# Kernel tuning notes

Measured on AMD Instinct MI355X. Metric: run time of the kernel, lower is better.

The kernel has to match this reference:

```python
import jax, jax.numpy as jnp
import numpy as np

HIDDEN = 1024
FEAT = 2048
BOTTLENECK = 512
B, T = 64, 512


def setup_inputs() -> dict:
    key = jax.random.key(0)
    k1, k2, k3, k4, k5 = jax.random.split(key, 5)
    hidden = jax.random.normal(k1, (B, HIDDEN), dtype=jnp.float32)
    feats = jax.random.normal(k2, (B, T, FEAT), dtype=jnp.float32)
    # nn.Linear weights stored as [out, in]; apply as x @ W.T
    W = jax.random.normal(k3, (BOTTLENECK, HIDDEN), dtype=jnp.float32) * (1.0 / np.sqrt(HIDDEN))
    U = jax.random.normal(k4, (BOTTLENECK, FEAT), dtype=jnp.float32) * (1.0 / np.sqrt(FEAT))
    b = jnp.ones((BOTTLENECK,), dtype=jnp.float32)
    w = jax.random.normal(k5, (1, BOTTLENECK), dtype=jnp.float32) * (1.0 / np.sqrt(BOTTLENECK))
    return {"hidden": hidden, "feats": feats, "W": W, "U": U, "b": b, "w": w}


def reference(hidden, feats, W, U, b, w):
    Wh = hidden @ W.T                      # [B, K]
    Uv = jnp.einsum('btf,kf->btk', feats, U)  # [B, T, K]
    e = jnp.tanh(Wh[:, None, :] + Uv + b)  # [B, T, K]
    energies = jnp.einsum('btk,ok->bto', e, w)  # [B, T, 1]
    weights = jax.nn.softmax(energies, axis=1)  # softmax over time
    attn_feats = jnp.sum(feats * weights, axis=1)  # [B, F]
    return attn_feats, weights
```

## Files before the change

kernel.cpp:

```cpp
#include <hip/hip_runtime.h>
#include <math.h>

#define BATCH 64
#define TDIM 512
#define FEAT 2048
#define HID 1024
#define KDIM 512
#define MROWS (BATCH * TDIM)
#define TCH 16
#define TCLEN (TDIM / TCH)

#define NSTEP (FEAT / 64)
#define TSLOT 2048
#define ASLOTS (128 * 32 * TSLOT)
#define BSLOTS (2 * 32 * TSLOT)

typedef __attribute__((ext_vector_type(8))) short short8;
typedef __attribute__((ext_vector_type(4))) float floatx4;

#define GLL16(g, l)                                                     \
    __builtin_amdgcn_global_load_lds(                                   \
        (const __attribute__((address_space(1))) void*)(g),             \
        (__attribute__((address_space(3))) void*)(l), 16, 0, 0)

#define VMWAIT(N) asm volatile("s_waitcnt vmcnt(" #N ")" ::: "memory")
#define SCHEDB    __builtin_amdgcn_sched_barrier(0)
#define SBAR      __builtin_amdgcn_s_barrier()

__device__ __forceinline__ unsigned short f2bf(float x) {
    unsigned int u = __float_as_uint(x);
    u += 0x7FFFu + ((u >> 16) & 1u);
    return (unsigned short)(u >> 16);
}

__global__ __launch_bounds__(256) void k0p(const float* __restrict__ feats,
                                           const float* __restrict__ U,
                                           const float* __restrict__ hidden,
                                           const float* __restrict__ W,
                                           const float* __restrict__ bias,
                                           unsigned short* __restrict__ Apk,
                                           unsigned short* __restrict__ Bpk,
                                           float* __restrict__ whb) {
    int bx = blockIdx.x;
    if (bx < 8192) {
        for (size_t gsl = (size_t)bx * 256 + threadIdx.x; gsl < ASLOTS;
             gsl += (size_t)8192 * 256) {
            int strip = (int)(gsl >> 16);
            int rem   = (int)(gsl & 65535);
            int tile  = rem >> 11;
            int s     = rem & 2047;
            int r     = s >> 3;
            int c     = (s & 7) ^ (r & 7);
            const float* src = feats + ((size_t)strip * 256 + r) * FEAT + tile * 64 + c * 8;
            float4 v0 = *(const float4*)src;
            float4 v1 = *(const float4*)(src + 4);
            ushort4 o0, o1;
            o0.x = f2bf(v0.x); o0.y = f2bf(v0.y); o0.z = f2bf(v0.z); o0.w = f2bf(v0.w);
            o1.x = f2bf(v1.x); o1.y = f2bf(v1.y); o1.z = f2bf(v1.z); o1.w = f2bf(v1.w);
            ((ushort4*)Apk)[gsl * 2]     = o0;
            ((ushort4*)Apk)[gsl * 2 + 1] = o1;
        }
    } else if (bx < 8704) {
        size_t gsl = (size_t)(bx - 8192) * 256 + threadIdx.x;
        int cb   = (int)(gsl >> 16);
        int rem  = (int)(gsl & 65535);
        int tile = rem >> 11;
        int s    = rem & 2047;
        int r    = s >> 3;
        int c    = (s & 7) ^ (r & 7);
        const float* src = U + ((size_t)cb * 256 + r) * FEAT + tile * 64 + c * 8;
        float4 v0 = *(const float4*)src;
        float4 v1 = *(const float4*)(src + 4);
        ushort4 o0, o1;
        o0.x = f2bf(v0.x); o0.y = f2bf(v0.y); o0.z = f2bf(v0.z); o0.w = f2bf(v0.w);
        o1.x = f2bf(v1.x); o1.y = f2bf(v1.y); o1.z = f2bf(v1.z); o1.w = f2bf(v1.w);
        ((ushort4*)Bpk)[gsl * 2]     = o0;
        ((ushort4*)Bpk)[gsl * 2 + 1] = o1;
    } else {
        int bid = bx - 8704;
        int b = bid >> 7;
        int k = (bid & 127) * 4 + (threadIdx.x >> 6);
        int lane = threadIdx.x & 63;
        const float* hrow = hidden + (size_t)b * HID;
        const float* wrow = W + (size_t)k * HID;
        float acc = 0.f;
        #pragma unroll 4
        for (int h = lane; h < HID; h += 64) acc += hrow[h] * wrow[h];
        #pragma unroll
        for (int off = 32; off > 0; off >>= 1) acc += __shfl_down(acc, off, 64);
        if (lane == 0) whb[b * KDIM + k] = acc + bias[k];
    }
}

__global__ __launch_bounds__(512, 2) void k2p(const unsigned short* __restrict__ Apk,
                                              const unsigned short* __restrict__ Bpk,
                                              const float* __restrict__ whb,
                                              const float* __restrict__ wvec,
                                              float* __restrict__ partial) {
    __shared__ __align__(16) unsigned short As[2][16384];
    __shared__ __align__(16) unsigned short Bs[2][16384];

    const int tid  = threadIdx.x;
    const int wave = tid >> 6;
    const int lane = tid & 63;
    const int wm = wave >> 2, wn = wave & 3;
    const int col = lane & 15, quad = lane >> 4;
    const int bx = blockIdx.x, by = blockIdx.y;

    const unsigned short* gA = Apk + (size_t)bx * (32 * TSLOT) * 8;
    const unsigned short* gB = Bpk + (size_t)by * (32 * TSLOT) * 8;

    #define STAGE(tt, hh, bb)                                                   \
        do {                                                                    \
            const int sbase_ = ((hh) & 1) * 1024 + wave * 128;                  \
            if ((hh) < 2) {                                                     \
                GLL16(gA + ((size_t)(tt) * TSLOT + sbase_) * 8 + lane * 8,      \
                      &As[bb][sbase_ * 8]);                                     \
                GLL16(gA + ((size_t)(tt) * TSLOT + sbase_ + 64) * 8 + lane * 8, \
                      &As[bb][(sbase_ + 64) * 8]);                              \
            } else {                                                            \
                GLL16(gB + ((size_t)(tt) * TSLOT + sbase_) * 8 + lane * 8,      \
                      &Bs[bb][sbase_ * 8]);                                     \
                GLL16(gB + ((size_t)(tt) * TSLOT + sbase_ + 64) * 8 + lane * 8, \
                      &Bs[bb][(sbase_ + 64) * 8]);                              \
            }                                                                   \
        } while (0)

    floatx4 acc[8][4];
    #pragma unroll
    for (int i = 0; i < 8; ++i)
        #pragma unroll
        for (int j = 0; j < 4; ++j) acc[i][j] = (floatx4){0.f, 0.f, 0.f, 0.f};

    #pragma unroll
    for (int h = 0; h < 4; ++h) STAGE(0, h, 0);

    short8 bf[4][2];
    for (int t = 0; t < NSTEP; ++t) {
        const int cb = t & 1, sb = cb ^ 1;
        #pragma unroll
        for (int p = 0; p < 4; ++p) {
            if (t < NSTEP - 1) STAGE(t + 1, p, sb);
            if (p == 0) {
                if (t < NSTEP - 1) { VMWAIT(2); } else { VMWAIT(0); }
                SCHEDB;
            }
            SBAR; SCHEDB;

            short8 af[2][2];
            #pragma unroll
            for (int i = 0; i < 2; ++i)
                #pragma unroll
                for (int kk = 0; kk < 2; ++kk) {
                    const int row = wm * 128 + (2 * p + i) * 16 + col;
                    af[i][kk] = *(const short8*)
                        &As[cb][(row * 8 + ((kk * 4 + quad) ^ (col & 7))) * 8];
                }
            if (p == 0) {
                #pragma unroll
                for (int j = 0; j < 4; ++j)
                    #pragma unroll
                    for (int kk = 0; kk < 2; ++kk) {
                        const int row = wn * 64 + j * 16 + col;
                        bf[j][kk] = *(const short8*)
                            &Bs[cb][(row * 8 + ((kk * 4 + quad) ^ (col & 7))) * 8];
                    }
            }
            __builtin_amdgcn_s_setprio(1);
            #pragma unroll
            for (int i = 0; i < 2; ++i)
                #pragma unroll
                for (int j = 0; j < 4; ++j)
                    #pragma unroll
                    for (int kk = 0; kk < 2; ++kk)
                        acc[2 * p + i][j] = __builtin_amdgcn_mfma_f32_16x16x32_bf16(
                            af[i][kk], bf[j][kk], acc[2 * p + i][j], 0, 0, 0);
            __builtin_amdgcn_s_setprio(0);
            SCHEDB; SBAR; SCHEDB;
        }
    }
    #undef STAGE

    __syncthreads();

    float (*sums)[256] = (float (*)[256])As;
    const int b = bx >> 1;
    float wk[4], hk[4];
    #pragma unroll
    for (int j = 0; j < 4; ++j) {
        const int k = by * 256 + wn * 64 + j * 16 + col;
        wk[j] = wvec[k];
        hk[j] = whb[b * KDIM + k];
    }
    #pragma unroll
    for (int i = 0; i < 8; ++i) {
        #pragma unroll
        for (int r = 0; r < 4; ++r) {
            float s = 0.f;
            #pragma unroll
            for (int j = 0; j < 4; ++j)
                s += tanhf(acc[i][j][r] + hk[j]) * wk[j];
            #pragma unroll
            for (int off = 8; off > 0; off >>= 1)
                s += __shfl_down(s, off, 16);
            if (col == 0)
                sums[wn][wm * 128 + i * 16 + quad * 4 + r] = s;
        }
    }
    __syncthreads();
    if (tid < 256)
        partial[(size_t)by * MROWS + bx * 256 + tid] =
            sums[0][tid] + sums[1][tid] + sums[2][tid] + sums[3][tid];
}

__global__ __launch_bounds__(512) void k3n(const float* __restrict__ partial,
                                           float* __restrict__ wout) {
    int b = blockIdx.x;
    int t = threadIdx.x;
    int idx = b * TDIM + t;
    float e = partial[idx] + partial[MROWS + idx];

    __shared__ float sm[512];
    sm[t] = e;
    __syncthreads();
    #pragma unroll
    for (int s = 256; s > 0; s >>= 1) {
        if (t < s) sm[t] = fmaxf(sm[t], sm[t + s]);
        __syncthreads();
    }
    float m = sm[0];
    __syncthreads();
    float ex = __expf(e - m);
    sm[t] = ex;
    __syncthreads();
    #pragma unroll
    for (int s = 256; s > 0; s >>= 1) {
        if (t < s) sm[t] += sm[t + s];
        __syncthreads();
    }
    float inv = 1.f / sm[0];
    wout[b * TDIM + t] = ex * inv;
}

__global__ __launch_bounds__(256) void k4p(const unsigned short* __restrict__ Apk,
                                           const float* __restrict__ weights,
                                           float* __restrict__ partial4) {
    int b  = blockIdx.y;
    int t0 = blockIdx.x * TCLEN;
    int tile = threadIdx.x >> 3;
    int ch   = threadIdx.x & 7;
    int f0   = tile * 64 + ch * 8;
    __shared__ float wsm[TCLEN];
    if (threadIdx.x < TCLEN) wsm[threadIdx.x] = weights[b * TDIM + t0 + threadIdx.x];
    __syncthreads();

    float a[8];
    #pragma unroll
    for (int e = 0; e < 8; ++e) a[e] = 0.f;
    #pragma unroll 4
    for (int t = 0; t < TCLEN; ++t) {
        int row = b * TDIM + t0 + t;
        int strip = row >> 8, r = row & 255;
        const short8 v = *(const short8*)(Apk +
            (((size_t)strip * 65536 + (size_t)tile * TSLOT + r * 8 + (ch ^ (r & 7))) * 8));
        float w = wsm[t];
        #pragma unroll
        for (int e = 0; e < 8; ++e)
            a[e] += __uint_as_float(((unsigned int)(unsigned short)v[e]) << 16) * w;
    }
    float* op = partial4 + ((size_t)blockIdx.x * BATCH + b) * FEAT + f0;
    float4 o0 = {a[0], a[1], a[2], a[3]};
    float4 o1 = {a[4], a[5], a[6], a[7]};
    *(float4*)op = o0;
    *(float4*)(op + 4) = o1;
}

__global__ __launch_bounds__(256) void k5_reduce(const float* __restrict__ partial4,
                                                 float* __restrict__ out) {
    int i4 = blockIdx.x * 256 + threadIdx.x;
    float4 s = ((const float4*)partial4)[i4];
    #pragma unroll
    for (int c = 1; c < TCH; ++c) {
        float4 v = ((const float4*)partial4)[(size_t)c * (BATCH * FEAT / 4) + i4];
        s.x += v.x; s.y += v.y; s.z += v.z; s.w += v.w;
    }
    ((float4*)out)[i4] = s;
}

#define BM 128
#define BN 128
#define BF 16
#define LDSPAD 4

__global__ __launch_bounds__(256) void k1_whb(const float* __restrict__ hidden,
                                              const float* __restrict__ W,
                                              const float* __restrict__ bias,
                                              float* __restrict__ whb) {
    int b = blockIdx.y;
    int k = blockIdx.x * 4 + (threadIdx.x >> 6);
    int lane = threadIdx.x & 63;
    const float* hrow = hidden + (size_t)b * HID;
    const float* wrow = W + (size_t)k * HID;
    float acc = 0.f;
    #pragma unroll 4
    for (int h = lane; h < HID; h += 64) acc += hrow[h] * wrow[h];
    #pragma unroll
    for (int off = 32; off > 0; off >>= 1) acc += __shfl_down(acc, off, 64);
    if (lane == 0) whb[b * KDIM + k] = acc + bias[k];
}

__global__ __launch_bounds__(256) void k2_energy(const float* __restrict__ feats,
                                                 const float* __restrict__ U,
                                                 const float* __restrict__ whb,
                                                 const float* __restrict__ wvec,
                                                 float* __restrict__ partial) {
    __shared__ __align__(16) float As[BF][BM + LDSPAD];
    __shared__ __align__(16) float Us[BF][BN + LDSPAD];

    const int row0 = blockIdx.x * BM;
    const int k0   = blockIdx.y * BN;
    const int tid  = threadIdx.x;
    const int tx   = tid & 15;
    const int ty   = tid >> 4;

    float acc[8][8];
    #pragma unroll
    for (int i = 0; i < 8; ++i)
        #pragma unroll
        for (int j = 0; j < 8; ++j) acc[i][j] = 0.f;

    for (int f0 = 0; f0 < FEAT; f0 += BF) {
        #pragma unroll
        for (int l = 0; l < 2; ++l) {
            int li = tid + l * 256;
            int r  = li >> 2;
            int c4 = (li & 3) * 4;
            float4 av = *(const float4*)(feats + (size_t)(row0 + r) * FEAT + f0 + c4);
            float4 uv = *(const float4*)(U     + (size_t)(k0   + r) * FEAT + f0 + c4);
            As[c4 + 0][r] = av.x; As[c4 + 1][r] = av.y;
            As[c4 + 2][r] = av.z; As[c4 + 3][r] = av.w;
            Us[c4 + 0][r] = uv.x; Us[c4 + 1][r] = uv.y;
            Us[c4 + 2][r] = uv.z; Us[c4 + 3][r] = uv.w;
        }
        __syncthreads();
        #pragma unroll
        for (int kf = 0; kf < BF; ++kf) {
            float4 a0 = *(const float4*)&As[kf][ty * 8];
            float4 a1 = *(const float4*)&As[kf][ty * 8 + 4];
            float4 u0 = *(const float4*)&Us[kf][tx * 8];
            float4 u1 = *(const float4*)&Us[kf][tx * 8 + 4];
            float a[8] = {a0.x, a0.y, a0.z, a0.w, a1.x, a1.y, a1.z, a1.w};
            float u[8] = {u0.x, u0.y, u0.z, u0.w, u1.x, u1.y, u1.z, u1.w};
            #pragma unroll
            for (int i = 0; i < 8; ++i)
                #pragma unroll
                for (int j = 0; j < 8; ++j) acc[i][j] += a[i] * u[j];
        }
        __syncthreads();
    }

    const int b = row0 >> 9;
    float psum[8];
    #pragma unroll
    for (int i = 0; i < 8; ++i) {
        float s = 0.f;
        #pragma unroll
        for (int j = 0; j < 8; ++j) {
            int k = k0 + tx * 8 + j;
            s += tanhf(acc[i][j] + whb[b * KDIM + k]) * wvec[k];
        }
        psum[i] = s;
    }
    #pragma unroll
    for (int off = 8; off > 0; off >>= 1)
        #pragma unroll
        for (int i = 0; i < 8; ++i) psum[i] += __shfl_down(psum[i], off, 16);

    if (tx == 0) {
        int c = blockIdx.y;
        #pragma unroll
        for (int i = 0; i < 8; ++i)
            partial[c * MROWS + row0 + ty * 8 + i] = psum[i];
    }
}

__global__ __launch_bounds__(512) void k3_softmax(const float* __restrict__ partial,
                                                  float* __restrict__ wout) {
    int b = blockIdx.x;
    int t = threadIdx.x;
    float e = 0.f;
    #pragma unroll
    for (int c = 0; c < 4; ++c) e += partial[c * MROWS + b * TDIM + t];

    __shared__ float sm[512];
    sm[t] = e;
    __syncthreads();
    #pragma unroll
    for (int s = 256; s > 0; s >>= 1) {
        if (t < s) sm[t] = fmaxf(sm[t], sm[t + s]);
        __syncthreads();
    }
    float m = sm[0];
    __syncthreads();
    float ex = __expf(e - m);
    sm[t] = ex;
    __syncthreads();
    #pragma unroll
    for (int s = 256; s > 0; s >>= 1) {
        if (t < s) sm[t] += sm[t + s];
        __syncthreads();
    }
    float inv = 1.f / sm[0];
    wout[b * TDIM + t] = ex * inv;
}

__global__ __launch_bounds__(256) void k4_direct(const float* __restrict__ feats,
                                                 const float* __restrict__ weights,
                                                 float* __restrict__ out) {
    int b = blockIdx.y;
    int f4 = (blockIdx.x * 256 + threadIdx.x) * 4;
    __shared__ float wsm[TDIM];
    wsm[threadIdx.x]       = weights[b * TDIM + threadIdx.x];
    wsm[threadIdx.x + 256] = weights[b * TDIM + 256 + threadIdx.x];
    __syncthreads();

    const float* fp = feats + (size_t)b * TDIM * FEAT + f4;
    float ax = 0.f, ay = 0.f, az = 0.f, aw = 0.f;
    for (int t = 0; t < TDIM; ++t) {
        float4 v = *(const float4*)(fp + (size_t)t * FEAT);
        float w = wsm[t];
        ax += v.x * w; ay += v.y * w; az += v.z * w; aw += v.w * w;
    }
    float4 o = {ax, ay, az, aw};
    *(float4*)(out + (size_t)b * FEAT + f4) = o;
}

extern "C" void kernel_launch(void* const* d_in, const int* in_sizes, int n_in,
                              void* d_out, int out_size, void* d_ws, size_t ws_size,
                              hipStream_t stream) {
    const float* hidden = (const float*)d_in[0];
    const float* feats  = (const float*)d_in[1];
    const float* W      = (const float*)d_in[2];
    const float* U      = (const float*)d_in[3];
    const float* bias   = (const float*)d_in[4];
    const float* wvec   = (const float*)d_in[5];

    float* out         = (float*)d_out;
    float* attn_out    = out;
    float* weights_out = out + (size_t)BATCH * FEAT;
    float* whb         = weights_out;
    float* partial     = attn_out;

    const size_t aBytes    = (size_t)ASLOTS * 16;
    const size_t bBytes    = (size_t)BSLOTS * 16;
    const size_t poolBytes = (size_t)TCH * BATCH * FEAT * sizeof(float);
    const bool fast = ws_size >= aBytes + bBytes + poolBytes;

    if (fast) {
        unsigned short* Apk = (unsigned short*)d_ws;
        unsigned short* Bpk = (unsigned short*)((char*)d_ws + aBytes);
        float* pool4 = (float*)((char*)d_ws + aBytes + bBytes);
        k0p<<<dim3(16896), 256, 0, stream>>>(feats, U, hidden, W, bias,
                                             Apk, Bpk, whb);
        k2p<<<dim3(128, 2), 512, 0, stream>>>(Apk, Bpk, whb, wvec, partial);
        k3n<<<dim3(BATCH), 512, 0, stream>>>(partial, weights_out);
        k4p<<<dim3(TCH, BATCH), 256, 0, stream>>>(Apk, weights_out, pool4);
        k5_reduce<<<dim3(BATCH * FEAT / 4 / 256), 256, 0, stream>>>(pool4, attn_out);
    } else {
        k1_whb<<<dim3(KDIM / 4, BATCH), 256, 0, stream>>>(hidden, W, bias, whb);
        k2_energy<<<dim3(MROWS / 128, KDIM / 128), 256, 0, stream>>>(
            feats, U, whb, wvec, partial);
        k3_softmax<<<dim3(BATCH), 512, 0, stream>>>(partial, weights_out);
        k4_direct<<<dim3(FEAT / 1024, BATCH), 256, 0, stream>>>(
            feats, weights_out, attn_out);
    }
}
```

Baseline: 532.4 us.

## Shrink energy GEMM tiles to 128x128 and replace partial-sum reduction with atomics

The bf16 packed layout moves from 256-row to 128-row strips, and the energy GEMM goes from a 512-thread 256x256 double-buffered pipelined kernel to a simpler 256-thread 128x128 single-buffered kernel on a 256x4 grid. Energy partials now live in workspace across four K-chunks, and k3n sums all four. The attention-pooling stage drops its separate reduction kernel: k4a atomically adds into the output, which k0p now zeroes. This trades the explicit load/compute overlap and larger reuse for more blocks and one fewer launch, at the cost of exposed load latency, extra B-tile traffic and atomic contention.

```diff
diff --git a/kernel.cpp b/kernel.cpp
--- a/kernel.cpp
+++ b/kernel.cpp
@@ -11,9 +11,9 @@
 #define TCLEN (TDIM / TCH)
 
 #define NSTEP (FEAT / 64)
-#define TSLOT 2048
-#define ASLOTS (128 * 32 * TSLOT)
-#define BSLOTS (2 * 32 * TSLOT)
+#define TSLOT 1024
+#define ASLOTS (256 * 32 * TSLOT)
+#define BSLOTS (4 * 32 * TSLOT)
 
 typedef __attribute__((ext_vector_type(8))) short short8;
 typedef __attribute__((ext_vector_type(4))) float floatx4;
@@ -22,10 +22,6 @@
     __builtin_amdgcn_global_load_lds(                                   \
         (const __attribute__((address_space(1))) void*)(g),             \
         (__attribute__((address_space(3))) void*)(l), 16, 0, 0)
-
-#define VMWAIT(N) asm volatile("s_waitcnt vmcnt(" #N ")" ::: "memory")
-#define SCHEDB    __builtin_amdgcn_sched_barrier(0)
-#define SBAR      __builtin_amdgcn_s_barrier()
 
 __device__ __forceinline__ unsigned short f2bf(float x) {
     unsigned int u = __float_as_uint(x);
@@ -40,18 +36,19 @@
                                            const float* __restrict__ bias,
                                            unsigned short* __restrict__ Apk,
                                            unsigned short* __restrict__ Bpk,
-                                           float* __restrict__ whb) {
+                                           float* __restrict__ whb,
+                                           float* __restrict__ attn_zero) {
     int bx = blockIdx.x;
     if (bx < 8192) {
         for (size_t gsl = (size_t)bx * 256 + threadIdx.x; gsl < ASLOTS;
              gsl += (size_t)8192 * 256) {
-            int strip = (int)(gsl >> 16);
-            int rem   = (int)(gsl & 65535);
-            int tile  = rem >> 11;
-            int s     = rem & 2047;
+            int strip = (int)(gsl >> 15);
+            int rem   = (int)(gsl & 32767);
+            int tile  = rem >> 10;
+            int s     = rem & 1023;
             int r     = s >> 3;
             int c     = (s & 7) ^ (r & 7);
-            const float* src = feats + ((size_t)strip * 256 + r) * FEAT + tile * 64 + c * 8;
+            const float* src = feats + ((size_t)strip * 128 + r) * FEAT + tile * 64 + c * 8;
             float4 v0 = *(const float4*)src;
             float4 v1 = *(const float4*)(src + 4);
             ushort4 o0, o1;
@@ -62,13 +59,13 @@
         }
     } else if (bx < 8704) {
         size_t gsl = (size_t)(bx - 8192) * 256 + threadIdx.x;
-        int cb   = (int)(gsl >> 16);
-        int rem  = (int)(gsl & 65535);
-        int tile = rem >> 11;
-        int s    = rem & 2047;
+        int kb   = (int)(gsl >> 15);
+        int rem  = (int)(gsl & 32767);
+        int tile = rem >> 10;
+        int s    = rem & 1023;
         int r    = s >> 3;
         int c    = (s & 7) ^ (r & 7);
-        const float* src = U + ((size_t)cb * 256 + r) * FEAT + tile * 64 + c * 8;
+        const float* src = U + ((size_t)kb * 128 + r) * FEAT + tile * 64 + c * 8;
         float4 v0 = *(const float4*)src;
         float4 v1 = *(const float4*)(src + 4);
         ushort4 o0, o1;
@@ -76,8 +73,11 @@
         o1.x = f2bf(v1.x); o1.y = f2bf(v1.y); o1.z = f2bf(v1.z); o1.w = f2bf(v1.w);
         ((ushort4*)Bpk)[gsl * 2]     = o0;
         ((ushort4*)Bpk)[gsl * 2 + 1] = o1;
+    } else if (bx < 8832) {
+        int i4 = (bx - 8704) * 256 + threadIdx.x;
+        ((float4*)attn_zero)[i4] = (float4){0.f, 0.f, 0.f, 0.f};
     } else {
-        int bid = bx - 8704;
+        int bid = bx - 8832;
         int b = bid >> 7;
         int k = (bid & 127) * 4 + (threadIdx.x >> 6);
         int lane = threadIdx.x & 63;
@@ -92,108 +92,72 @@
     }
 }
 
-__global__ __launch_bounds__(512, 2) void k2p(const unsigned short* __restrict__ Apk,
-                                              const unsigned short* __restrict__ Bpk,
-                                              const float* __restrict__ whb,
-                                              const float* __restrict__ wvec,
-                                              float* __restrict__ partial) {
-    __shared__ __align__(16) unsigned short As[2][16384];
-    __shared__ __align__(16) unsigned short Bs[2][16384];
+__global__ __launch_bounds__(256) void k2m(const unsigned short* __restrict__ Apk,
+                                           const unsigned short* __restrict__ Bpk,
+                                           const float* __restrict__ whb,
+                                           const float* __restrict__ wvec,
+                                           float* __restrict__ partial) {
+    __shared__ __align__(16) unsigned short As[TSLOT * 8];
+    __shared__ __align__(16) unsigned short Bs[TSLOT * 8];
 
     const int tid  = threadIdx.x;
     const int wave = tid >> 6;
     const int lane = tid & 63;
-    const int wm = wave >> 2, wn = wave & 3;
+    const int wm = wave >> 1, wn = wave & 1;
     const int col = lane & 15, quad = lane >> 4;
-    const int bx = blockIdx.x, by = blockIdx.y;
-
-    const unsigned short* gA = Apk + (size_t)bx * (32 * TSLOT) * 8;
-    const unsigned short* gB = Bpk + (size_t)by * (32 * TSLOT) * 8;
-
-    #define STAGE(tt, hh, bb)                                                   \
-        do {                                                                    \
-            const int sbase_ = ((hh) & 1) * 1024 + wave * 128;                  \
-            if ((hh) < 2) {                                                     \
-                GLL16(gA + ((size_t)(tt) * TSLOT + sbase_) * 8 + lane * 8,      \
-                      &As[bb][sbase_ * 8]);                                     \
-                GLL16(gA + ((size_t)(tt) * TSLOT + sbase_ + 64) * 8 + lane * 8, \
-                      &As[bb][(sbase_ + 64) * 8]);                              \
-            } else {                                                            \
-                GLL16(gB + ((size_t)(tt) * TSLOT + sbase_) * 8 + lane * 8,      \
-                      &Bs[bb][sbase_ * 8]);                                     \
-                GLL16(gB + ((size_t)(tt) * TSLOT + sbase_ + 64) * 8 + lane * 8, \
-                      &Bs[bb][(sbase_ + 64) * 8]);                              \
-            }                                                                   \
-        } while (0)
-
-    floatx4 acc[8][4];
-    #pragma unroll
-    for (int i = 0; i < 8; ++i)
+    const int bx = blockIdx.x;
+    const int kb = blockIdx.y;
+
+    const unsigned short* gA = Apk + ((size_t)bx * (32 * TSLOT) + wave * 256 + lane) * 8;
+    const unsigned short* gB = Bpk + ((size_t)kb * (32 * TSLOT) + wave * 256 + lane) * 8;
+    unsigned short* lA = As + (wave * 256) * 8;
+    unsigned short* lB = Bs + (wave * 256) * 8;
+
+    floatx4 acc[4][4];
+    #pragma unroll
+    for (int i = 0; i < 4; ++i)
         #pragma unroll
         for (int j = 0; j < 4; ++j) acc[i][j] = (floatx4){0.f, 0.f, 0.f, 0.f};
 
-    #pragma unroll
-    for (int h = 0; h < 4; ++h) STAGE(0, h, 0);
-
-    short8 bf[4][2];
     for (int t = 0; t < NSTEP; ++t) {
-        const int cb = t & 1, sb = cb ^ 1;
-        #pragma unroll
-        for (int p = 0; p < 4; ++p) {
-            if (t < NSTEP - 1) STAGE(t + 1, p, sb);
-            if (p == 0) {
-                if (t < NSTEP - 1) { VMWAIT(2); } else { VMWAIT(0); }
-                SCHEDB;
-            }
-            SBAR; SCHEDB;
-
-            short8 af[2][2];
-            #pragma unroll
-            for (int i = 0; i < 2; ++i)
-                #pragma unroll
-                for (int kk = 0; kk < 2; ++kk) {
-                    const int row = wm * 128 + (2 * p + i) * 16 + col;
-                    af[i][kk] = *(const short8*)
-                        &As[cb][(row * 8 + ((kk * 4 + quad) ^ (col & 7))) * 8];
-                }
-            if (p == 0) {
+        #pragma unroll
+        for (int g = 0; g < 4; ++g) {
+            GLL16(gA + (size_t)(t * 1024 + g * 64) * 8, lA + g * 64 * 8);
+            GLL16(gB + (size_t)(t * 1024 + g * 64) * 8, lB + g * 64 * 8);
+        }
+        __syncthreads();
+
+        #pragma unroll
+        for (int kk = 0; kk < 2; ++kk) {
+            const int sw = (kk * 4 + quad) ^ (col & 7);
+            short8 af[4], bf[4];
+            #pragma unroll
+            for (int i = 0; i < 4; ++i)
+                af[i] = *(const short8*)&As[((wm * 64 + i * 16 + col) * 8 + sw) * 8];
+            #pragma unroll
+            for (int j = 0; j < 4; ++j)
+                bf[j] = *(const short8*)&Bs[((wn * 64 + j * 16 + col) * 8 + sw) * 8];
+            #pragma unroll
+            for (int i = 0; i < 4; ++i)
                 #pragma unroll
                 for (int j = 0; j < 4; ++j)
-                    #pragma unroll
-                    for (int kk = 0; kk < 2; ++kk) {
-                        const int row = wn * 64 + j * 16 + col;
-                        bf[j][kk] = *(const short8*)
-                            &Bs[cb][(row * 8 + ((kk * 4 + quad) ^ (col & 7))) * 8];
-                    }
-            }
-            __builtin_amdgcn_s_setprio(1);
-            #pragma unroll
-            for (int i = 0; i < 2; ++i)
-                #pragma unroll
-                for (int j = 0; j < 4; ++j)
-                    #pragma unroll
-                    for (int kk = 0; kk < 2; ++kk)
-                        acc[2 * p + i][j] = __builtin_amdgcn_mfma_f32_16x16x32_bf16(
-                            af[i][kk], bf[j][kk], acc[2 * p + i][j], 0, 0, 0);
-            __builtin_amdgcn_s_setprio(0);
-            SCHEDB; SBAR; SCHEDB;
-        }
-    }
-    #undef STAGE
-
-    __syncthreads();
-
-    float (*sums)[256] = (float (*)[256])As;
-    const int b = bx >> 1;
+                    acc[i][j] = __builtin_amdgcn_mfma_f32_16x16x32_bf16(
+                        af[i], bf[j], acc[i][j], 0, 0, 0);
+        }
+        __syncthreads();
+    }
+
+    float (*sums)[128] = (float (*)[128])As;
+    const int b = bx >> 2;
     float wk[4], hk[4];
     #pragma unroll
     for (int j = 0; j < 4; ++j) {
-        const int k = by * 256 + wn * 64 + j * 16 + col;
+        const int k = kb * 128 + wn * 64 + j * 16 + col;
         wk[j] = wvec[k];
         hk[j] = whb[b * KDIM + k];
     }
     #pragma unroll
-    for (int i = 0; i < 8; ++i) {
+    for (int i = 0; i < 4; ++i) {
         #pragma unroll
         for (int r = 0; r < 4; ++r) {
             float s = 0.f;
@@ -204,13 +168,13 @@
             for (int off = 8; off > 0; off >>= 1)
                 s += __shfl_down(s, off, 16);
             if (col == 0)
-                sums[wn][wm * 128 + i * 16 + quad * 4 + r] = s;
-        }
-    }
-    __syncthreads();
-    if (tid < 256)
-        partial[(size_t)by * MROWS + bx * 256 + tid] =
-            sums[0][tid] + sums[1][tid] + sums[2][tid] + sums[3][tid];
+                sums[wn][wm * 64 + i * 16 + quad * 4 + r] = s;
+        }
+    }
+    __syncthreads();
+    if (tid < 128)
+        partial[(size_t)kb * MROWS + bx * 128 + tid] =
+            sums[0][tid] + sums[1][tid];
 }
 
 __global__ __launch_bounds__(512) void k3n(const float* __restrict__ partial,
@@ -218,7 +182,8 @@
     int b = blockIdx.x;
     int t = threadIdx.x;
     int idx = b * TDIM + t;
-    float e = partial[idx] + partial[MROWS + idx];
+    float e = partial[idx] + partial[MROWS + idx] +
+              partial[2 * MROWS + idx] + partial[3 * MROWS + idx];
 
     __shared__ float sm[512];
     sm[t] = e;
@@ -242,9 +207,9 @@
     wout[b * TDIM + t] = ex * inv;
 }
 
-__global__ __launch_bounds__(256) void k4p(const unsigned short* __restrict__ Apk,
+__global__ __launch_bounds__(256) void k4a(const unsigned short* __restrict__ Apk,
                                            const float* __restrict__ weights,
-                                           float* __restrict__ partial4) {
+                                           float* __restrict__ attn_out) {
     int b  = blockIdx.y;
     int t0 = blockIdx.x * TCLEN;
     int tile = threadIdx.x >> 3;
@@ -260,31 +225,17 @@
     #pragma unroll 4
     for (int t = 0; t < TCLEN; ++t) {
         int row = b * TDIM + t0 + t;
-        int strip = row >> 8, r = row & 255;
+        int strip = row >> 7, r = row & 127;
         const short8 v = *(const short8*)(Apk +
-            (((size_t)strip * 65536 + (size_t)tile * TSLOT + r * 8 + (ch ^ (r & 7))) * 8));
+            (((size_t)strip * 32768 + (size_t)tile * TSLOT + r * 8 + (ch ^ (r & 7))) * 8));
         float w = wsm[t];
         #pragma unroll
         for (int e = 0; e < 8; ++e)
             a[e] += __uint_as_float(((unsigned int)(unsigned short)v[e]) << 16) * w;
     }
-    float* op = partial4 + ((size_t)blockIdx.x * BATCH + b) * FEAT + f0;
-    float4 o0 = {a[0], a[1], a[2], a[3]};
-    float4 o1 = {a[4], a[5], a[6], a[7]};
-    *(float4*)op = o0;
-    *(float4*)(op + 4) = o1;
-}
-
-__global__ __launch_bounds__(256) void k5_reduce(const float* __restrict__ partial4,
-                                                 float* __restrict__ out) {
-    int i4 = blockIdx.x * 256 + threadIdx.x;
-    float4 s = ((const float4*)partial4)[i4];
-    #pragma unroll
-    for (int c = 1; c < TCH; ++c) {
-        float4 v = ((const float4*)partial4)[(size_t)c * (BATCH * FEAT / 4) + i4];
-        s.x += v.x; s.y += v.y; s.z += v.z; s.w += v.w;
-    }
-    ((float4*)out)[i4] = s;
+    float* op = attn_out + (size_t)b * FEAT + f0;
+    #pragma unroll
+    for (int e = 0; e < 8; ++e) atomicAdd(op + e, a[e]);
 }
 
 #define BM 128
@@ -449,24 +400,23 @@
     float* attn_out    = out;
     float* weights_out = out + (size_t)BATCH * FEAT;
     float* whb         = weights_out;
-    float* partial     = attn_out;
 
     const size_t aBytes    = (size_t)ASLOTS * 16;
     const size_t bBytes    = (size_t)BSLOTS * 16;
-    const size_t poolBytes = (size_t)TCH * BATCH * FEAT * sizeof(float);
-    const bool fast = ws_size >= aBytes + bBytes + poolBytes;
+    const size_t pBytes    = (size_t)4 * MROWS * sizeof(float);
+    const bool fast = ws_size >= aBytes + bBytes + pBytes;
 
     if (fast) {
         unsigned short* Apk = (unsigned short*)d_ws;
         unsigned short* Bpk = (unsigned short*)((char*)d_ws + aBytes);
-        float* pool4 = (float*)((char*)d_ws + aBytes + bBytes);
-        k0p<<<dim3(16896), 256, 0, stream>>>(feats, U, hidden, W, bias,
-                                             Apk, Bpk, whb);
-        k2p<<<dim3(128, 2), 512, 0, stream>>>(Apk, Bpk, whb, wvec, partial);
+        float* partial = (float*)((char*)d_ws + aBytes + bBytes);
+        k0p<<<dim3(17024), 256, 0, stream>>>(feats, U, hidden, W, bias,
+                                             Apk, Bpk, whb, attn_out);
+        k2m<<<dim3(256, 4), 256, 0, stream>>>(Apk, Bpk, whb, wvec, partial);
         k3n<<<dim3(BATCH), 512, 0, stream>>>(partial, weights_out);
-        k4p<<<dim3(TCH, BATCH), 256, 0, stream>>>(Apk, weights_out, pool4);
-        k5_reduce<<<dim3(BATCH * FEAT / 4 / 256), 256, 0, stream>>>(pool4, attn_out);
+        k4a<<<dim3(TCH, BATCH), 256, 0, stream>>>(Apk, weights_out, attn_out);
     } else {
+        float* partial = attn_out;
         k1_whb<<<dim3(KDIM / 4, BATCH), 256, 0, stream>>>(hidden, W, bias, whb);
         k2_energy<<<dim3(MROWS / 128, KDIM / 128), 256, 0, stream>>>(
             feats, U, whb, wvec, partial);
```

Measured after the change: 568.3 us. 1.07x slower.
